# Optimization experiments

Measured on AMD Instinct MI355X. Metric: run time of the kernel, lower is better.

Reference implementation:

```python
import jax, jax.numpy as jnp
import numpy as np

B, S, D, H = 4, 2048, 1024, 16
DK = D // H  # d_k = d_v = 64


def setup_inputs() -> dict:
    key = jax.random.key(0)
    ks = jax.random.split(key, 9)
    sc = 0.02
    return {
        "x": jax.random.normal(ks[0], (B, S, D), dtype=jnp.float32),
        "Wq": jax.random.normal(ks[1], (H, D, DK), dtype=jnp.float32) * sc,
        "bq": jax.random.normal(ks[2], (H, DK), dtype=jnp.float32) * sc,
        "Wk": jax.random.normal(ks[3], (H, D, DK), dtype=jnp.float32) * sc,
        "bk": jax.random.normal(ks[4], (H, DK), dtype=jnp.float32) * sc,
        "Wv": jax.random.normal(ks[5], (H, D, DK), dtype=jnp.float32) * sc,
        "bv": jax.random.normal(ks[6], (H, DK), dtype=jnp.float32) * sc,
        "Wo": jax.random.normal(ks[7], (D, D), dtype=jnp.float32) * sc,
        "bo": jax.random.normal(ks[8], (D,), dtype=jnp.float32) * sc,
    }


def reference(x, Wq, bq, Wk, bk, Wv, bv, Wo, bo):
    # per-head learned projections (heads stacked on leading axis h)
    Q = jnp.einsum("bsd,hdk->bhsk", x, Wq) + bq[None, :, None, :]
    K = jnp.einsum("bsd,hdk->bhsk", x, Wk) + bk[None, :, None, :]
    V = jnp.einsum("bsd,hdk->bhsk", x, Wv) + bv[None, :, None, :]
    scores = jnp.einsum("bhsk,bhtk->bhst", Q, K) / jnp.sqrt(jnp.float32(DK))
    # causal mask: future_sight=0, past_sight=None -> positions t > s replaced by -1e9
    s_idx = jnp.arange(S)
    causal = s_idx[:, None] >= s_idx[None, :]  # [S, S] True where allowed
    scores = jnp.where(causal[None, None, :, :], scores, jnp.float32(-1e9))
    attn = jax.nn.softmax(scores, axis=-1)
    out = jnp.einsum("bhst,bhtk->bhsk", attn, V)  # [B, H, S, DK]
    # concat heads along feature dim (head order matches ModuleList order)
    cat = out.transpose(0, 2, 1, 3).reshape(B, S, D)
    return cat @ Wo + bo
```

## Files before the change

### kernel.cpp

```cpp
#include <hip/hip_runtime.h>
#include <stdint.h>

#define B_  4
#define S_  2048
#define D_  1024
#define H_  16
#define DK_ 64
#define M_  (B_ * S_)

typedef __attribute__((ext_vector_type(8))) short bf16x8;
typedef __attribute__((ext_vector_type(4))) float f32x4;

#define QSCALE 0.1803368801111204f

__device__ __forceinline__ uint16_t f2bf(float f) {
    uint32_t u = __builtin_bit_cast(uint32_t, f);
    u = (u + 0x7FFFu + ((u >> 16) & 1u)) >> 16;
    return (uint16_t)u;
}

__device__ __forceinline__ uint32_t pk2bf(float hi, float lo) {
    uint32_t a = __builtin_bit_cast(uint32_t, hi) + 0x8000u;
    uint32_t b = __builtin_bit_cast(uint32_t, lo) + 0x8000u;
    return __builtin_amdgcn_perm(a, b, 0x07060302u);
}

__global__ __launch_bounds__(256) void cvt_bf16_kernel(const float* __restrict__ in,
                                                       uint16_t* __restrict__ out, int n) {
    int i = (blockIdx.x * 256 + threadIdx.x) * 8;
    if (i >= n) return;
    float4 a = *(const float4*)&in[i];
    float4 b = *(const float4*)&in[i + 4];
    uint16_t o[8] = {f2bf(a.x), f2bf(a.y), f2bf(a.z), f2bf(a.w),
                     f2bf(b.x), f2bf(b.y), f2bf(b.z), f2bf(b.w)};
    *(uint4*)&out[i] = *(const uint4*)o;
}

__global__ __launch_bounds__(256) void transpose_cvt_qkv_kernel(
    const float* __restrict__ Wq, const float* __restrict__ Wk,
    const float* __restrict__ Wv, uint16_t* __restrict__ Wt) {
    __shared__ __align__(16) uint16_t tile[64][72];
    const int z = blockIdx.z;
    const int sel = z >> 4, mat = z & 15;
    const float* base = (sel == 0) ? Wq : (sel == 1) ? Wk : Wv;
    const float* inm = base + (size_t)mat * 1024 * 64;
    uint16_t* outm = Wt + (size_t)z * 65536;
    const int r0 = blockIdx.x * 64;
    const int t = threadIdx.x;
    const int lr = t >> 2, lc = (t & 3) * 16;
    uint16_t tmp[16];
    #pragma unroll
    for (int j = 0; j < 16; j += 4) {
        float4 v = *(const float4*)&inm[(size_t)(r0 + lr) * 64 + lc + j];
        tmp[j] = f2bf(v.x); tmp[j + 1] = f2bf(v.y); tmp[j + 2] = f2bf(v.z); tmp[j + 3] = f2bf(v.w);
    }
    *(uint4*)&tile[lr][lc]     = ((const uint4*)tmp)[0];
    *(uint4*)&tile[lr][lc + 8] = ((const uint4*)tmp)[1];
    __syncthreads();
    const int oc = t >> 2, orr = (t & 3) * 16;
    uint16_t ot[16];
    #pragma unroll
    for (int j = 0; j < 16; ++j) ot[j] = tile[orr + j][oc];
    *(uint4*)&outm[(size_t)oc * 1024 + r0 + orr]     = ((const uint4*)ot)[0];
    *(uint4*)&outm[(size_t)oc * 1024 + r0 + orr + 8] = ((const uint4*)ot)[1];
}

__global__ __launch_bounds__(256) void transpose_cvt_kernel(
    const float* __restrict__ in, uint16_t* __restrict__ out, int R, int C) {
    __shared__ __align__(16) uint16_t tile[64][72];
    const float* inm = in;
    uint16_t* outm = out;
    const int r0 = blockIdx.x * 64, c0 = blockIdx.y * 64;
    const int t = threadIdx.x;
    const int lr = t >> 2, lc = (t & 3) * 16;
    uint16_t tmp[16];
    #pragma unroll
    for (int j = 0; j < 16; j += 4) {
        float4 v = *(const float4*)&inm[(size_t)(r0 + lr) * C + c0 + lc + j];
        tmp[j] = f2bf(v.x); tmp[j + 1] = f2bf(v.y); tmp[j + 2] = f2bf(v.z); tmp[j + 3] = f2bf(v.w);
    }
    *(uint4*)&tile[lr][lc]     = ((const uint4*)tmp)[0];
    *(uint4*)&tile[lr][lc + 8] = ((const uint4*)tmp)[1];
    __syncthreads();
    const int oc = t >> 2, orr = (t & 3) * 16;
    uint16_t ot[16];
    #pragma unroll
    for (int j = 0; j < 16; ++j) ot[j] = tile[orr + j][oc];
    *(uint4*)&outm[(size_t)(c0 + oc) * R + r0 + orr]     = ((const uint4*)ot)[0];
    *(uint4*)&outm[(size_t)(c0 + oc) * R + r0 + orr + 8] = ((const uint4*)ot)[1];
}

__global__ __launch_bounds__(256) void qkv_mfma_kernel(
    const uint16_t* __restrict__ xb, const uint16_t* __restrict__ Wt,
    const float* __restrict__ bq, const float* __restrict__ bk, const float* __restrict__ bv,
    uint16_t* __restrict__ Q, uint16_t* __restrict__ K, uint16_t* __restrict__ V)
{
    __shared__ __align__(16) uint16_t As[128][72];
    __shared__ __align__(16) uint16_t Bs[128][72];
    const int tid = threadIdx.x;
    const int nb = blockIdx.x;
    const int sel = nb >> 3, npair = nb & 7;
    const int m0 = blockIdx.y * 128;
    const int lane = tid & 63, w = tid >> 6;
    const int wr = w >> 1, wc = w & 1;
    const int ll = lane & 15, quad = lane >> 4;

    const uint16_t* Bg = Wt + (size_t)nb * 128 * 1024;
    const float* bias = (sel == 0) ? bq : (sel == 1) ? bk : bv;

    const int ar = tid >> 1, ac = (tid & 1) * 32;

    f32x4 acc[4][4];
    const f32x4 zz = {0.f, 0.f, 0.f, 0.f};
    #pragma unroll
    for (int i = 0; i < 4; ++i)
        #pragma unroll
        for (int j = 0; j < 4; ++j) acc[i][j] = zz;

    for (int k0 = 0; k0 < 1024; k0 += 64) {
        __syncthreads();
        const uint16_t* ag = &xb[(size_t)(m0 + ar) * 1024 + k0 + ac];
        uint4 a0 = *(const uint4*)(ag);
        uint4 a1 = *(const uint4*)(ag + 8);
        uint4 a2 = *(const uint4*)(ag + 16);
        uint4 a3 = *(const uint4*)(ag + 24);
        const uint16_t* bg = &Bg[(size_t)ar * 1024 + k0 + ac];
        uint4 b0 = *(const uint4*)(bg);
        uint4 b1 = *(const uint4*)(bg + 8);
        uint4 b2 = *(const uint4*)(bg + 16);
        uint4 b3 = *(const uint4*)(bg + 24);
        *(uint4*)&As[ar][ac]      = a0;
        *(uint4*)&As[ar][ac + 8]  = a1;
        *(uint4*)&As[ar][ac + 16] = a2;
        *(uint4*)&As[ar][ac + 24] = a3;
        *(uint4*)&Bs[ar][ac]      = b0;
        *(uint4*)&Bs[ar][ac + 8]  = b1;
        *(uint4*)&Bs[ar][ac + 16] = b2;
        *(uint4*)&Bs[ar][ac + 24] = b3;
        __syncthreads();
        #pragma unroll
        for (int ks = 0; ks < 2; ++ks) {
            bf16x8 af[4], bfv[4];
            #pragma unroll
            for (int mt = 0; mt < 4; ++mt)
                af[mt] = *(const bf16x8*)&As[wr * 64 + mt * 16 + ll][ks * 32 + quad * 8];
            #pragma unroll
            for (int nt = 0; nt < 4; ++nt)
                bfv[nt] = *(const bf16x8*)&Bs[wc * 64 + nt * 16 + ll][ks * 32 + quad * 8];
            #pragma unroll
            for (int mt = 0; mt < 4; ++mt)
                #pragma unroll
                for (int nt = 0; nt < 4; ++nt)
                    acc[mt][nt] = __builtin_amdgcn_mfma_f32_16x16x32_bf16(af[mt], bfv[nt], acc[mt][nt], 0, 0, 0);
        }
    }

    if (sel == 2) {
        #pragma unroll
        for (int nt = 0; nt < 4; ++nt) {
            const int nl = wc * 64 + nt * 16 + ll;
            const int hh = npair * 2 + (nl >> 6);
            const int dk = nl & 63;
            const float bval = bias[npair * 128 + nl];
            #pragma unroll
            for (int mt = 0; mt < 4; ++mt) {
                int m = m0 + wr * 64 + mt * 16 + quad * 4;
                int b = m >> 11, s = m & 2047;
                uint2 pv;
                pv.x = pk2bf(acc[mt][nt][1] + bval, acc[mt][nt][0] + bval);
                pv.y = pk2bf(acc[mt][nt][3] + bval, acc[mt][nt][2] + bval);
                *(uint2*)&V[((size_t)(b * 16 + hh) * 64 + dk) * 2048 + s] = pv;
            }
        }
    } else {
        uint16_t* Out = (sel == 0) ? Q : K;
        const float qs = (sel == 0) ? QSCALE : 1.0f;
        #pragma unroll
        for (int nt = 0; nt < 4; ++nt) {
            const int nl = wc * 64 + nt * 16 + ll;
            const int hh = npair * 2 + (nl >> 6);
            const int dk = nl & 63;
            const float bval = bias[npair * 128 + nl];
            #pragma unroll
            for (int mt = 0; mt < 4; ++mt) {
                #pragma unroll
                for (int r = 0; r < 4; ++r) {
                    int m = m0 + wr * 64 + mt * 16 + quad * 4 + r;
                    int b = m >> 11, s = m & 2047;
                    float v = (acc[mt][nt][r] + bval) * qs;
                    Out[((size_t)(b * 16 + hh) * 2048 + s) * 64 + dk] = f2bf(v);
                }
            }
        }
    }
}

__global__ __launch_bounds__(256) void attn_mfma_kernel(
    const uint16_t* __restrict__ Q, const uint16_t* __restrict__ K,
    const uint16_t* __restrict__ Vg, uint16_t* __restrict__ CAT)
{
    __shared__ __align__(16) uint16_t Ks[64][72];
    __shared__ __align__(16) uint16_t Vt[64][72];
    __shared__ __align__(16) uint16_t Ps[128][72];

    const int tid = threadIdx.x;
    const int lane = tid & 63, w = tid >> 6;
    const int ll = lane & 15, quad = lane >> 4;
    const int p = blockIdx.x;
    const int bh = blockIdx.y;
    const int b = bh >> 4, h = bh & 15;

    const uint16_t* Qbh = Q + (size_t)bh * S_ * 64;
    const uint16_t* Kbh = K + (size_t)bh * S_ * 64;
    const uint16_t* Vbh = Vg + (size_t)bh * 64 * S_;
    uint16_t* Cbh = CAT + (size_t)b * 2048 * 1024 + h * 64;

    const int sr = tid >> 2, sc = (tid & 3) * 16;

    bf16x8 onesf;
    #pragma unroll
    for (int j = 0; j < 8; ++j) onesf[j] = (ll == 0) ? (short)0x3F80 : (short)0;

    const f32x4 zz = {0.f, 0.f, 0.f, 0.f};

    #pragma unroll 1
    for (int phase = 0; phase < 2; ++phase) {
        const int qtb = (phase == 0) ? (15 - p) : p;
        const int q0 = qtb * 128;
        const int qw = q0 + w * 32;

        bf16x8 qf[2][2];
        #pragma unroll
        for (int mt = 0; mt < 2; ++mt)
            #pragma unroll
            for (int ks = 0; ks < 2; ++ks)
                qf[mt][ks] = *(const bf16x8*)&Qbh[(size_t)(qw + mt * 16 + ll) * 64 + ks * 32 + quad * 8];

        f32x4 oacc[2][4];
        f32x4 lacc[2];
        #pragma unroll
        for (int i = 0; i < 2; ++i) {
            lacc[i] = zz;
            #pragma unroll
            for (int j = 0; j < 4; ++j) oacc[i][j] = zz;
        }

        const int ktmax = 2 * qtb + 1;

        for (int kt = 0; kt <= ktmax; ++kt) {
            const int tb = kt * 64;
            __syncthreads();
            {
                const uint16_t* g = &Kbh[(size_t)(tb + sr) * 64 + sc];
                uint4 v0 = *(const uint4*)g, v1 = *(const uint4*)(g + 8);
                *(uint4*)&Ks[sr][sc] = v0;
                *(uint4*)&Ks[sr][sc + 8] = v1;
            }
            {
                const uint16_t* g = &Vbh[(size_t)sr * 2048 + tb + sc];
                uint4 v0 = *(const uint4*)g, v1 = *(const uint4*)(g + 8);
                *(uint4*)&Vt[sr][sc] = v0;
                *(uint4*)&Vt[sr][sc + 8] = v1;
            }
            __syncthreads();

            const bool active = (tb <= qw + 31);
            if (active) {
                f32x4 sacc[4][2];
                #pragma unroll
                for (int i = 0; i < 4; ++i)
                    #pragma unroll
                    for (int j = 0; j < 2; ++j) sacc[i][j] = zz;
                #pragma unroll
                for (int ks = 0; ks < 2; ++ks) {
                    #pragma unroll
                    for (int tt = 0; tt < 4; ++tt) {
                        bf16x8 kf = *(const bf16x8*)&Ks[tt * 16 + ll][ks * 32 + quad * 8];
                        #pragma unroll
                        for (int mt = 0; mt < 2; ++mt)
                            sacc[tt][mt] = __builtin_amdgcn_mfma_f32_16x16x32_bf16(kf, qf[mt][ks], sacc[tt][mt], 0, 0, 0);
                    }
                }

                const bool needMask = (tb + 63 > qw);
                #pragma unroll
                for (int mt = 0; mt < 2; ++mt) {
                    const int qg = qw + mt * 16 + ll;
                    #pragma unroll
                    for (int tt = 0; tt < 4; ++tt) {
                        #pragma unroll
                        for (int r = 0; r < 4; ++r) {
                            float v = sacc[tt][mt][r];
                            if (needMask) {
                                int tg = tb + tt * 16 + quad * 4 + r;
                                v = (tg > qg) ? -1e30f : v;
                            }
                            sacc[tt][mt][r] = __builtin_amdgcn_exp2f(v);
                        }
                        uint2 pv;
                        pv.x = pk2bf(sacc[tt][mt][1], sacc[tt][mt][0]);
                        pv.y = pk2bf(sacc[tt][mt][3], sacc[tt][mt][2]);
                        *(uint2*)&Ps[w * 32 + mt * 16 + ll][tt * 16 + quad * 4] = pv;
                    }
                }

                #pragma unroll
                for (int ks = 0; ks < 2; ++ks) {
                    bf16x8 pf[2], vf[4];
                    #pragma unroll
                    for (int mt = 0; mt < 2; ++mt)
                        pf[mt] = *(const bf16x8*)&Ps[w * 32 + mt * 16 + ll][ks * 32 + quad * 8];
                    #pragma unroll
                    for (int nt = 0; nt < 4; ++nt)
                        vf[nt] = *(const bf16x8*)&Vt[nt * 16 + ll][ks * 32 + quad * 8];
                    #pragma unroll
                    for (int mt = 0; mt < 2; ++mt) {
                        lacc[mt] = __builtin_amdgcn_mfma_f32_16x16x32_bf16(pf[mt], onesf, lacc[mt], 0, 0, 0);
                        #pragma unroll
                        for (int nt = 0; nt < 4; ++nt)
                            oacc[mt][nt] = __builtin_amdgcn_mfma_f32_16x16x32_bf16(pf[mt], vf[nt], oacc[mt][nt], 0, 0, 0);
                    }
                }
            }
        }

        #pragma unroll
        for (int mt = 0; mt < 2; ++mt) {
            f32x4 li;
            #pragma unroll
            for (int r = 0; r < 4; ++r)
                li[r] = 1.0f / __shfl(lacc[mt][r], lane & 48);
            #pragma unroll
            for (int r = 0; r < 4; ++r) {
                int q = qw + mt * 16 + quad * 4 + r;
                #pragma unroll
                for (int nt = 0; nt < 4; ++nt) {
                    float v = oacc[mt][nt][r] * li[r];
                    Cbh[(size_t)q * 1024 + nt * 16 + ll] = f2bf(v);
                }
            }
        }
    }
}

__global__ __launch_bounds__(256) void oproj_mfma_kernel(
    const uint16_t* __restrict__ CATb, const uint16_t* __restrict__ Wot,
    const float* __restrict__ bo, float* __restrict__ out)
{
    __shared__ __align__(16) uint16_t As[128][72];
    __shared__ __align__(16) uint16_t Bs[128][72];
    const int tid = threadIdx.x;
    const int n0 = blockIdx.x * 128;
    const int m0 = blockIdx.y * 128;
    const int lane = tid & 63, w = tid >> 6;
    const int wr = w >> 1, wc = w & 1;
    const int ll = lane & 15, quad = lane >> 4;

    const int ar = tid >> 1, ac = (tid & 1) * 32;

    f32x4 acc[4][4];
    const f32x4 zz = {0.f, 0.f, 0.f, 0.f};
    #pragma unroll
    for (int i = 0; i < 4; ++i)
        #pragma unroll
        for (int j = 0; j < 4; ++j) acc[i][j] = zz;

    for (int k0 = 0; k0 < 1024; k0 += 64) {
        __syncthreads();
        const uint16_t* ag = &CATb[(size_t)(m0 + ar) * 1024 + k0 + ac];
        uint4 a0 = *(const uint4*)(ag);
        uint4 a1 = *(const uint4*)(ag + 8);
        uint4 a2 = *(const uint4*)(ag + 16);
        uint4 a3 = *(const uint4*)(ag + 24);
        const uint16_t* bg = &Wot[(size_t)(n0 + ar) * 1024 + k0 + ac];
        uint4 b0 = *(const uint4*)(bg);
        uint4 b1 = *(const uint4*)(bg + 8);
        uint4 b2 = *(const uint4*)(bg + 16);
        uint4 b3 = *(const uint4*)(bg + 24);
        *(uint4*)&As[ar][ac]      = a0;
        *(uint4*)&As[ar][ac + 8]  = a1;
        *(uint4*)&As[ar][ac + 16] = a2;
        *(uint4*)&As[ar][ac + 24] = a3;
        *(uint4*)&Bs[ar][ac]      = b0;
        *(uint4*)&Bs[ar][ac + 8]  = b1;
        *(uint4*)&Bs[ar][ac + 16] = b2;
        *(uint4*)&Bs[ar][ac + 24] = b3;
        __syncthreads();
        #pragma unroll
        for (int ks = 0; ks < 2; ++ks) {
            bf16x8 af[4], bfv[4];
            #pragma unroll
            for (int mt = 0; mt < 4; ++mt)
                af[mt] = *(const bf16x8*)&As[wr * 64 + mt * 16 + ll][ks * 32 + quad * 8];
            #pragma unroll
            for (int nt = 0; nt < 4; ++nt)
                bfv[nt] = *(const bf16x8*)&Bs[wc * 64 + nt * 16 + ll][ks * 32 + quad * 8];
            #pragma unroll
            for (int mt = 0; mt < 4; ++mt)
                #pragma unroll
                for (int nt = 0; nt < 4; ++nt)
                    acc[mt][nt] = __builtin_amdgcn_mfma_f32_16x16x32_bf16(af[mt], bfv[nt], acc[mt][nt], 0, 0, 0);
        }
    }

    #pragma unroll
    for (int nt = 0; nt < 4; ++nt) {
        const int nl = wc * 64 + nt * 16 + ll;
        const float bval = bo[n0 + nl];
        #pragma unroll
        for (int mt = 0; mt < 4; ++mt) {
            #pragma unroll
            for (int r = 0; r < 4; ++r) {
                int m = m0 + wr * 64 + mt * 16 + quad * 4 + r;
                out[(size_t)m * 1024 + n0 + nl] = acc[mt][nt][r] + bval;
            }
        }
    }
}

extern "C" void kernel_launch(void* const* d_in, const int* in_sizes, int n_in,
                              void* d_out, int out_size, void* d_ws, size_t ws_size,
                              hipStream_t stream) {
    const float* x  = (const float*)d_in[0];
    const float* Wq = (const float*)d_in[1];
    const float* bq = (const float*)d_in[2];
    const float* Wk = (const float*)d_in[3];
    const float* bk = (const float*)d_in[4];
    const float* Wv = (const float*)d_in[5];
    const float* bv = (const float*)d_in[6];
    const float* Wo = (const float*)d_in[7];
    const float* bo = (const float*)d_in[8];

    uint8_t* p = (uint8_t*)d_ws;
    uint16_t* xb   = (uint16_t*)p; p += (size_t)M_ * D_ * 2;
    uint16_t* Wt   = (uint16_t*)p; p += (size_t)3 * H_ * DK_ * D_ * 2;
    uint16_t* Wot  = (uint16_t*)p; p += (size_t)D_ * D_ * 2;
    uint16_t* Qb   = (uint16_t*)p; p += (size_t)B_ * H_ * S_ * DK_ * 2;
    uint16_t* Kb   = (uint16_t*)p; p += (size_t)B_ * H_ * S_ * DK_ * 2;
    uint16_t* Vb   = (uint16_t*)p; p += (size_t)B_ * H_ * S_ * DK_ * 2;
    uint16_t* CATb = (uint16_t*)p;

    cvt_bf16_kernel<<<dim3((M_ * D_) / 2048), 256, 0, stream>>>(x, xb, M_ * D_);
    transpose_cvt_qkv_kernel<<<dim3(16, 1, 48), 256, 0, stream>>>(Wq, Wk, Wv, Wt);
    transpose_cvt_kernel<<<dim3(D_ / 64, D_ / 64, 1), 256, 0, stream>>>(Wo, Wot, D_, D_);

    qkv_mfma_kernel<<<dim3(24, M_ / 128), 256, 0, stream>>>(xb, Wt, bq, bk, bv, Qb, Kb, Vb);
    attn_mfma_kernel<<<dim3(8, B_ * H_), 256, 0, stream>>>(Qb, Kb, Vb, CATb);
    oproj_mfma_kernel<<<dim3(8, M_ / 128), 256, 0, stream>>>(CATb, Wot, bo, (float*)d_out);
}
```

Baseline: 289.9 us.

## Use direct global-to-LDS loads, prefragmented weights, swizzled LDS, and one-tile attention blocks

Weights are repacked once into MFMA fragment order so each GEMM wave reads its B operand straight from global memory into registers, with no LDS staging for B. Activation, K and V tiles are loaded with global_load_lds into an XOR-swizzled LDS layout, which removes the register round trip and the padding. The attention grid changes from 8 blocks that each handle a paired short and long query tile to 16 blocks that each handle one tile, giving more parallelism but unbalanced per-block work. The risks are uncoalesced strided reads in the repack kernels and causal load imbalance across blocks.

```diff
diff --git a/kernel.cpp b/kernel.cpp
--- a/kernel.cpp
+++ b/kernel.cpp
@@ -23,6 +23,12 @@
     uint32_t a = __builtin_bit_cast(uint32_t, hi) + 0x8000u;
     uint32_t b = __builtin_bit_cast(uint32_t, lo) + 0x8000u;
     return __builtin_amdgcn_perm(a, b, 0x07060302u);
+}
+
+__device__ __forceinline__ void gl2lds16(const void* g, void* l) {
+    __builtin_amdgcn_global_load_lds(
+        (const __attribute__((address_space(1))) uint32_t*)g,
+        (__attribute__((address_space(3))) uint32_t*)l, 16, 0, 0);
 }
 
 __global__ __launch_bounds__(256) void cvt_bf16_kernel(const float* __restrict__ in,
@@ -36,67 +42,52 @@
     *(uint4*)&out[i] = *(const uint4*)o;
 }
 
-__global__ __launch_bounds__(256) void transpose_cvt_qkv_kernel(
+__global__ __launch_bounds__(256) void frag_qkv_kernel(
     const float* __restrict__ Wq, const float* __restrict__ Wk,
-    const float* __restrict__ Wv, uint16_t* __restrict__ Wt) {
-    __shared__ __align__(16) uint16_t tile[64][72];
-    const int z = blockIdx.z;
-    const int sel = z >> 4, mat = z & 15;
-    const float* base = (sel == 0) ? Wq : (sel == 1) ? Wk : Wv;
-    const float* inm = base + (size_t)mat * 1024 * 64;
-    uint16_t* outm = Wt + (size_t)z * 65536;
-    const int r0 = blockIdx.x * 64;
-    const int t = threadIdx.x;
-    const int lr = t >> 2, lc = (t & 3) * 16;
-    uint16_t tmp[16];
-    #pragma unroll
-    for (int j = 0; j < 16; j += 4) {
-        float4 v = *(const float4*)&inm[(size_t)(r0 + lr) * 64 + lc + j];
-        tmp[j] = f2bf(v.x); tmp[j + 1] = f2bf(v.y); tmp[j + 2] = f2bf(v.z); tmp[j + 3] = f2bf(v.w);
-    }
-    *(uint4*)&tile[lr][lc]     = ((const uint4*)tmp)[0];
-    *(uint4*)&tile[lr][lc + 8] = ((const uint4*)tmp)[1];
-    __syncthreads();
-    const int oc = t >> 2, orr = (t & 3) * 16;
-    uint16_t ot[16];
-    #pragma unroll
-    for (int j = 0; j < 16; ++j) ot[j] = tile[orr + j][oc];
-    *(uint4*)&outm[(size_t)oc * 1024 + r0 + orr]     = ((const uint4*)ot)[0];
-    *(uint4*)&outm[(size_t)oc * 1024 + r0 + orr + 8] = ((const uint4*)ot)[1];
-}
-
-__global__ __launch_bounds__(256) void transpose_cvt_kernel(
-    const float* __restrict__ in, uint16_t* __restrict__ out, int R, int C) {
-    __shared__ __align__(16) uint16_t tile[64][72];
-    const float* inm = in;
-    uint16_t* outm = out;
-    const int r0 = blockIdx.x * 64, c0 = blockIdx.y * 64;
-    const int t = threadIdx.x;
-    const int lr = t >> 2, lc = (t & 3) * 16;
-    uint16_t tmp[16];
-    #pragma unroll
-    for (int j = 0; j < 16; j += 4) {
-        float4 v = *(const float4*)&inm[(size_t)(r0 + lr) * C + c0 + lc + j];
-        tmp[j] = f2bf(v.x); tmp[j + 1] = f2bf(v.y); tmp[j + 2] = f2bf(v.z); tmp[j + 3] = f2bf(v.w);
-    }
-    *(uint4*)&tile[lr][lc]     = ((const uint4*)tmp)[0];
-    *(uint4*)&tile[lr][lc + 8] = ((const uint4*)tmp)[1];
-    __syncthreads();
-    const int oc = t >> 2, orr = (t & 3) * 16;
-    uint16_t ot[16];
-    #pragma unroll
-    for (int j = 0; j < 16; ++j) ot[j] = tile[orr + j][oc];
-    *(uint4*)&outm[(size_t)(c0 + oc) * R + r0 + orr]     = ((const uint4*)ot)[0];
-    *(uint4*)&outm[(size_t)(c0 + oc) * R + r0 + orr + 8] = ((const uint4*)ot)[1];
+    const float* __restrict__ Wv, uint16_t* __restrict__ Wtf) {
+    const int kb = blockIdx.x;
+    const int nb = blockIdx.y;
+    const int sel = nb >> 3, npair = nb & 7;
+    const float* W = (sel == 0) ? Wq : (sel == 1) ? Wk : Wv;
+    const int lane = threadIdx.x & 63, w = threadIdx.x >> 6;
+    const int ll = lane & 15, quad = lane >> 4;
+    #pragma unroll
+    for (int i = 0; i < 2; ++i) {
+        const int ntg = w + i * 4;
+        const int nl = ntg * 16 + ll;
+        const int h = npair * 2 + (nl >> 6), dk = nl & 63;
+        const float* src = W + ((size_t)h * 1024 + kb * 32 + quad * 8) * 64 + dk;
+        uint16_t tmp[8];
+        #pragma unroll
+        for (int j = 0; j < 8; ++j) tmp[j] = f2bf(src[(size_t)j * 64]);
+        *(uint4*)&Wtf[((((size_t)nb * 8 + ntg) * 32 + kb) * 64 + lane) * 8] = *(const uint4*)tmp;
+    }
+}
+
+__global__ __launch_bounds__(256) void frag_wo_kernel(
+    const float* __restrict__ Wo, uint16_t* __restrict__ Wof) {
+    const int kb = blockIdx.x;
+    const int nb2 = blockIdx.y;
+    const int lane = threadIdx.x & 63, w = threadIdx.x >> 6;
+    const int ll = lane & 15, quad = lane >> 4;
+    #pragma unroll
+    for (int i = 0; i < 2; ++i) {
+        const int ntg = w + i * 4;
+        const int n = nb2 * 128 + ntg * 16 + ll;
+        const float* src = Wo + (size_t)(kb * 32 + quad * 8) * 1024 + n;
+        uint16_t tmp[8];
+        #pragma unroll
+        for (int j = 0; j < 8; ++j) tmp[j] = f2bf(src[(size_t)j * 1024]);
+        *(uint4*)&Wof[((((size_t)nb2 * 8 + ntg) * 32 + kb) * 64 + lane) * 8] = *(const uint4*)tmp;
+    }
 }
 
 __global__ __launch_bounds__(256) void qkv_mfma_kernel(
-    const uint16_t* __restrict__ xb, const uint16_t* __restrict__ Wt,
+    const uint16_t* __restrict__ xb, const uint16_t* __restrict__ Wtf,
     const float* __restrict__ bq, const float* __restrict__ bk, const float* __restrict__ bv,
     uint16_t* __restrict__ Q, uint16_t* __restrict__ K, uint16_t* __restrict__ V)
 {
-    __shared__ __align__(16) uint16_t As[128][72];
-    __shared__ __align__(16) uint16_t Bs[128][72];
+    __shared__ uint16_t As[128 * 64];
     const int tid = threadIdx.x;
     const int nb = blockIdx.x;
     const int sel = nb >> 3, npair = nb & 7;
@@ -104,11 +95,13 @@
     const int lane = tid & 63, w = tid >> 6;
     const int wr = w >> 1, wc = w & 1;
     const int ll = lane & 15, quad = lane >> 4;
-
-    const uint16_t* Bg = Wt + (size_t)nb * 128 * 1024;
     const float* bias = (sel == 0) ? bq : (sel == 1) ? bk : bv;
 
-    const int ar = tid >> 1, ac = (tid & 1) * 32;
+    const int sr8 = lane >> 3;
+    const int scb = (lane & 7) ^ sr8;
+    uint16_t* aL = As + (size_t)(w * 4) * 512;
+
+    const size_t bfbase = (size_t)nb * 8 * 32 * 512 + (size_t)lane * 8;
 
     f32x4 acc[4][4];
     const f32x4 zz = {0.f, 0.f, 0.f, 0.f};
@@ -119,39 +112,31 @@
 
     for (int k0 = 0; k0 < 1024; k0 += 64) {
         __syncthreads();
-        const uint16_t* ag = &xb[(size_t)(m0 + ar) * 1024 + k0 + ac];
-        uint4 a0 = *(const uint4*)(ag);
-        uint4 a1 = *(const uint4*)(ag + 8);
-        uint4 a2 = *(const uint4*)(ag + 16);
-        uint4 a3 = *(const uint4*)(ag + 24);
-        const uint16_t* bg = &Bg[(size_t)ar * 1024 + k0 + ac];
-        uint4 b0 = *(const uint4*)(bg);
-        uint4 b1 = *(const uint4*)(bg + 8);
-        uint4 b2 = *(const uint4*)(bg + 16);
-        uint4 b3 = *(const uint4*)(bg + 24);
-        *(uint4*)&As[ar][ac]      = a0;
-        *(uint4*)&As[ar][ac + 8]  = a1;
-        *(uint4*)&As[ar][ac + 16] = a2;
-        *(uint4*)&As[ar][ac + 24] = a3;
-        *(uint4*)&Bs[ar][ac]      = b0;
-        *(uint4*)&Bs[ar][ac + 8]  = b1;
-        *(uint4*)&Bs[ar][ac + 16] = b2;
-        *(uint4*)&Bs[ar][ac + 24] = b3;
+        #pragma unroll
+        for (int i = 0; i < 4; ++i)
+            gl2lds16(xb + (size_t)(m0 + w * 32 + i * 8 + sr8) * 1024 + k0 + scb * 8,
+                     aL + i * 512);
+        bf16x8 bfv[2][4];
+        const int kb = k0 >> 5;
+        #pragma unroll
+        for (int ks = 0; ks < 2; ++ks)
+            #pragma unroll
+            for (int nt = 0; nt < 4; ++nt)
+                bfv[ks][nt] = *(const bf16x8*)&Wtf[bfbase + ((size_t)(wc * 4 + nt) * 32 + kb + ks) * 512];
         __syncthreads();
         #pragma unroll
         for (int ks = 0; ks < 2; ++ks) {
-            bf16x8 af[4], bfv[4];
+            bf16x8 af[4];
+            #pragma unroll
+            for (int mt = 0; mt < 4; ++mt) {
+                const int row = wr * 64 + mt * 16 + ll;
+                af[mt] = *(const bf16x8*)&As[row * 64 + (((ks * 4 + quad) ^ (ll & 7)) * 8)];
+            }
             #pragma unroll
             for (int mt = 0; mt < 4; ++mt)
-                af[mt] = *(const bf16x8*)&As[wr * 64 + mt * 16 + ll][ks * 32 + quad * 8];
-            #pragma unroll
-            for (int nt = 0; nt < 4; ++nt)
-                bfv[nt] = *(const bf16x8*)&Bs[wc * 64 + nt * 16 + ll][ks * 32 + quad * 8];
-            #pragma unroll
-            for (int mt = 0; mt < 4; ++mt)
                 #pragma unroll
                 for (int nt = 0; nt < 4; ++nt)
-                    acc[mt][nt] = __builtin_amdgcn_mfma_f32_16x16x32_bf16(af[mt], bfv[nt], acc[mt][nt], 0, 0, 0);
+                    acc[mt][nt] = __builtin_amdgcn_mfma_f32_16x16x32_bf16(af[mt], bfv[ks][nt], acc[mt][nt], 0, 0, 0);
         }
     }
 
@@ -199,14 +184,14 @@
     const uint16_t* __restrict__ Q, const uint16_t* __restrict__ K,
     const uint16_t* __restrict__ Vg, uint16_t* __restrict__ CAT)
 {
-    __shared__ __align__(16) uint16_t Ks[64][72];
-    __shared__ __align__(16) uint16_t Vt[64][72];
-    __shared__ __align__(16) uint16_t Ps[128][72];
+    __shared__ uint16_t Ks[64 * 64];
+    __shared__ uint16_t Vt[64 * 64];
+    __shared__ __align__(16) uint16_t Ps[128][68];
 
     const int tid = threadIdx.x;
     const int lane = tid & 63, w = tid >> 6;
     const int ll = lane & 15, quad = lane >> 4;
-    const int p = blockIdx.x;
+    const int qtb = 15 - (int)blockIdx.x;
     const int bh = blockIdx.y;
     const int b = bh >> 4, h = bh & 15;
 
@@ -215,148 +200,145 @@
     const uint16_t* Vbh = Vg + (size_t)bh * 64 * S_;
     uint16_t* Cbh = CAT + (size_t)b * 2048 * 1024 + h * 64;
 
-    const int sr = tid >> 2, sc = (tid & 3) * 16;
+    const int q0 = qtb * 128;
+    const int qw = q0 + w * 32;
+
+    const int sr8 = lane >> 3;
+    const int scb = (lane & 7) ^ sr8;
 
     bf16x8 onesf;
     #pragma unroll
     for (int j = 0; j < 8; ++j) onesf[j] = (ll == 0) ? (short)0x3F80 : (short)0;
 
+    bf16x8 qf[2][2];
+    #pragma unroll
+    for (int mt = 0; mt < 2; ++mt)
+        #pragma unroll
+        for (int ks = 0; ks < 2; ++ks)
+            qf[mt][ks] = *(const bf16x8*)&Qbh[(size_t)(qw + mt * 16 + ll) * 64 + ks * 32 + quad * 8];
+
     const f32x4 zz = {0.f, 0.f, 0.f, 0.f};
-
-    #pragma unroll 1
-    for (int phase = 0; phase < 2; ++phase) {
-        const int qtb = (phase == 0) ? (15 - p) : p;
-        const int q0 = qtb * 128;
-        const int qw = q0 + w * 32;
-
-        bf16x8 qf[2][2];
-        #pragma unroll
-        for (int mt = 0; mt < 2; ++mt)
-            #pragma unroll
-            for (int ks = 0; ks < 2; ++ks)
-                qf[mt][ks] = *(const bf16x8*)&Qbh[(size_t)(qw + mt * 16 + ll) * 64 + ks * 32 + quad * 8];
-
-        f32x4 oacc[2][4];
-        f32x4 lacc[2];
+    f32x4 oacc[2][4];
+    f32x4 lacc[2];
+    #pragma unroll
+    for (int i = 0; i < 2; ++i) {
+        lacc[i] = zz;
+        #pragma unroll
+        for (int j = 0; j < 4; ++j) oacc[i][j] = zz;
+    }
+
+    const int ktmax = 2 * qtb + 1;
+
+    for (int kt = 0; kt <= ktmax; ++kt) {
+        const int tb = kt * 64;
+        __syncthreads();
         #pragma unroll
         for (int i = 0; i < 2; ++i) {
-            lacc[i] = zz;
-            #pragma unroll
-            for (int j = 0; j < 4; ++j) oacc[i][j] = zz;
-        }
-
-        const int ktmax = 2 * qtb + 1;
-
-        for (int kt = 0; kt <= ktmax; ++kt) {
-            const int tb = kt * 64;
-            __syncthreads();
-            {
-                const uint16_t* g = &Kbh[(size_t)(tb + sr) * 64 + sc];
-                uint4 v0 = *(const uint4*)g, v1 = *(const uint4*)(g + 8);
-                *(uint4*)&Ks[sr][sc] = v0;
-                *(uint4*)&Ks[sr][sc + 8] = v1;
-            }
-            {
-                const uint16_t* g = &Vbh[(size_t)sr * 2048 + tb + sc];
-                uint4 v0 = *(const uint4*)g, v1 = *(const uint4*)(g + 8);
-                *(uint4*)&Vt[sr][sc] = v0;
-                *(uint4*)&Vt[sr][sc + 8] = v1;
-            }
-            __syncthreads();
-
-            const bool active = (tb <= qw + 31);
-            if (active) {
-                f32x4 sacc[4][2];
-                #pragma unroll
-                for (int i = 0; i < 4; ++i)
-                    #pragma unroll
-                    for (int j = 0; j < 2; ++j) sacc[i][j] = zz;
-                #pragma unroll
-                for (int ks = 0; ks < 2; ++ks) {
-                    #pragma unroll
-                    for (int tt = 0; tt < 4; ++tt) {
-                        bf16x8 kf = *(const bf16x8*)&Ks[tt * 16 + ll][ks * 32 + quad * 8];
-                        #pragma unroll
-                        for (int mt = 0; mt < 2; ++mt)
-                            sacc[tt][mt] = __builtin_amdgcn_mfma_f32_16x16x32_bf16(kf, qf[mt][ks], sacc[tt][mt], 0, 0, 0);
-                    }
-                }
-
-                const bool needMask = (tb + 63 > qw);
-                #pragma unroll
-                for (int mt = 0; mt < 2; ++mt) {
-                    const int qg = qw + mt * 16 + ll;
-                    #pragma unroll
-                    for (int tt = 0; tt < 4; ++tt) {
-                        #pragma unroll
-                        for (int r = 0; r < 4; ++r) {
-                            float v = sacc[tt][mt][r];
-                            if (needMask) {
-                                int tg = tb + tt * 16 + quad * 4 + r;
-                                v = (tg > qg) ? -1e30f : v;
-                            }
-                            sacc[tt][mt][r] = __builtin_amdgcn_exp2f(v);
-                        }
-                        uint2 pv;
-                        pv.x = pk2bf(sacc[tt][mt][1], sacc[tt][mt][0]);
-                        pv.y = pk2bf(sacc[tt][mt][3], sacc[tt][mt][2]);
-                        *(uint2*)&Ps[w * 32 + mt * 16 + ll][tt * 16 + quad * 4] = pv;
-                    }
-                }
-
-                #pragma unroll
-                for (int ks = 0; ks < 2; ++ks) {
-                    bf16x8 pf[2], vf[4];
+            const int c = w * 2 + i;
+            const int row = c * 8 + sr8;
+            gl2lds16(Kbh + (size_t)(tb + row) * 64 + scb * 8, Ks + (size_t)c * 512);
+            gl2lds16(Vbh + (size_t)row * 2048 + tb + scb * 8, Vt + (size_t)c * 512);
+        }
+        __syncthreads();
+
+        const bool active = (tb <= qw + 31);
+        if (active) {
+            f32x4 sacc[4][2];
+            #pragma unroll
+            for (int i = 0; i < 4; ++i)
+                #pragma unroll
+                for (int j = 0; j < 2; ++j) sacc[i][j] = zz;
+            #pragma unroll
+            for (int ks = 0; ks < 2; ++ks) {
+                #pragma unroll
+                for (int tt = 0; tt < 4; ++tt) {
+                    const int row = tt * 16 + ll;
+                    bf16x8 kf = *(const bf16x8*)&Ks[row * 64 + (((ks * 4 + quad) ^ (ll & 7)) * 8)];
                     #pragma unroll
                     for (int mt = 0; mt < 2; ++mt)
-                        pf[mt] = *(const bf16x8*)&Ps[w * 32 + mt * 16 + ll][ks * 32 + quad * 8];
+                        sacc[tt][mt] = __builtin_amdgcn_mfma_f32_16x16x32_bf16(kf, qf[mt][ks], sacc[tt][mt], 0, 0, 0);
+                }
+            }
+
+            const bool needMask = (tb + 63 > qw);
+            #pragma unroll
+            for (int mt = 0; mt < 2; ++mt) {
+                const int qg = qw + mt * 16 + ll;
+                #pragma unroll
+                for (int tt = 0; tt < 4; ++tt) {
+                    #pragma unroll
+                    for (int r = 0; r < 4; ++r) {
+                        float v = sacc[tt][mt][r];
+                        if (needMask) {
+                            int tg = tb + tt * 16 + quad * 4 + r;
+                            v = (tg > qg) ? -1e30f : v;
+                        }
+                        sacc[tt][mt][r] = __builtin_amdgcn_exp2f(v);
+                    }
+                    uint2 pv;
+                    pv.x = pk2bf(sacc[tt][mt][1], sacc[tt][mt][0]);
+                    pv.y = pk2bf(sacc[tt][mt][3], sacc[tt][mt][2]);
+                    *(uint2*)&Ps[w * 32 + mt * 16 + ll][tt * 16 + quad * 4] = pv;
+                }
+            }
+
+            #pragma unroll
+            for (int ks = 0; ks < 2; ++ks) {
+                bf16x8 pf[2], vf[4];
+                #pragma unroll
+                for (int mt = 0; mt < 2; ++mt)
+                    pf[mt] = *(const bf16x8*)&Ps[w * 32 + mt * 16 + ll][ks * 32 + quad * 8];
+                #pragma unroll
+                for (int nt = 0; nt < 4; ++nt) {
+                    const int row = nt * 16 + ll;
+                    vf[nt] = *(const bf16x8*)&Vt[row * 64 + (((ks * 4 + quad) ^ (ll & 7)) * 8)];
+                }
+                #pragma unroll
+                for (int mt = 0; mt < 2; ++mt) {
+                    lacc[mt] = __builtin_amdgcn_mfma_f32_16x16x32_bf16(pf[mt], onesf, lacc[mt], 0, 0, 0);
                     #pragma unroll
                     for (int nt = 0; nt < 4; ++nt)
-                        vf[nt] = *(const bf16x8*)&Vt[nt * 16 + ll][ks * 32 + quad * 8];
-                    #pragma unroll
-                    for (int mt = 0; mt < 2; ++mt) {
-                        lacc[mt] = __builtin_amdgcn_mfma_f32_16x16x32_bf16(pf[mt], onesf, lacc[mt], 0, 0, 0);
-                        #pragma unroll
-                        for (int nt = 0; nt < 4; ++nt)
-                            oacc[mt][nt] = __builtin_amdgcn_mfma_f32_16x16x32_bf16(pf[mt], vf[nt], oacc[mt][nt], 0, 0, 0);
-                    }
+                        oacc[mt][nt] = __builtin_amdgcn_mfma_f32_16x16x32_bf16(pf[mt], vf[nt], oacc[mt][nt], 0, 0, 0);
                 }
             }
         }
-
-        #pragma unroll
-        for (int mt = 0; mt < 2; ++mt) {
-            f32x4 li;
-            #pragma unroll
-            for (int r = 0; r < 4; ++r)
-                li[r] = 1.0f / __shfl(lacc[mt][r], lane & 48);
-            #pragma unroll
-            for (int r = 0; r < 4; ++r) {
-                int q = qw + mt * 16 + quad * 4 + r;
-                #pragma unroll
-                for (int nt = 0; nt < 4; ++nt) {
-                    float v = oacc[mt][nt][r] * li[r];
-                    Cbh[(size_t)q * 1024 + nt * 16 + ll] = f2bf(v);
-                }
+    }
+
+    #pragma unroll
+    for (int mt = 0; mt < 2; ++mt) {
+        f32x4 li;
+        #pragma unroll
+        for (int r = 0; r < 4; ++r)
+            li[r] = 1.0f / __shfl(lacc[mt][r], lane & 48);
+        #pragma unroll
+        for (int r = 0; r < 4; ++r) {
+            int q = qw + mt * 16 + quad * 4 + r;
+            #pragma unroll
+            for (int nt = 0; nt < 4; ++nt) {
+                float v = oacc[mt][nt][r] * li[r];
+                Cbh[(size_t)q * 1024 + nt * 16 + ll] = f2bf(v);
             }
         }
     }
 }
 
 __global__ __launch_bounds__(256) void oproj_mfma_kernel(
-    const uint16_t* __restrict__ CATb, const uint16_t* __restrict__ Wot,
+    const uint16_t* __restrict__ CATb, const uint16_t* __restrict__ Wof,
     const float* __restrict__ bo, float* __restrict__ out)
 {
-    __shared__ __align__(16) uint16_t As[128][72];
-    __shared__ __align__(16) uint16_t Bs[128][72];
+    __shared__ uint16_t As[128 * 64];
     const int tid = threadIdx.x;
-    const int n0 = blockIdx.x * 128;
+    const int nb2 = blockIdx.x;
     const int m0 = blockIdx.y * 128;
     const int lane = tid & 63, w = tid >> 6;
     const int wr = w >> 1, wc = w & 1;
     const int ll = lane & 15, quad = lane >> 4;
 
-    const int ar = tid >> 1, ac = (tid & 1) * 32;
+    const int sr8 = lane >> 3;
+    const int scb = (lane & 7) ^ sr8;
+    uint16_t* aL = As + (size_t)(w * 4) * 512;
+
+    const size_t bfbase = (size_t)nb2 * 8 * 32 * 512 + (size_t)lane * 8;
 
     f32x4 acc[4][4];
     const f32x4 zz = {0.f, 0.f, 0.f, 0.f};
@@ -367,52 +349,44 @@
 
     for (int k0 = 0; k0 < 1024; k0 += 64) {
         __syncthreads();
-        const uint16_t* ag = &CATb[(size_t)(m0 + ar) * 1024 + k0 + ac];
-        uint4 a0 = *(const uint4*)(ag);
-        uint4 a1 = *(const uint4*)(ag + 8);
-        uint4 a2 = *(const uint4*)(ag + 16);
-        uint4 a3 = *(const uint4*)(ag + 24);
-        const uint16_t* bg = &Wot[(size_t)(n0 + ar) * 1024 + k0 + ac];
-        uint4 b0 = *(const uint4*)(bg);
-        uint4 b1 = *(const uint4*)(bg + 8);
-        uint4 b2 = *(const uint4*)(bg + 16);
-        uint4 b3 = *(const uint4*)(bg + 24);
-        *(uint4*)&As[ar][ac]      = a0;
-        *(uint4*)&As[ar][ac + 8]  = a1;
-        *(uint4*)&As[ar][ac + 16] = a2;
-        *(uint4*)&As[ar][ac + 24] = a3;
-        *(uint4*)&Bs[ar][ac]      = b0;
-        *(uint4*)&Bs[ar][ac + 8]  = b1;
-        *(uint4*)&Bs[ar][ac + 16] = b2;
-        *(uint4*)&Bs[ar][ac + 24] = b3;
+        #pragma unroll
+        for (int i = 0; i < 4; ++i)
+            gl2lds16(CATb + (size_t)(m0 + w * 32 + i * 8 + sr8) * 1024 + k0 + scb * 8,
+                     aL + i * 512);
+        bf16x8 bfv[2][4];
+        const int kb = k0 >> 5;
+        #pragma unroll
+        for (int ks = 0; ks < 2; ++ks)
+            #pragma unroll
+            for (int nt = 0; nt < 4; ++nt)
+                bfv[ks][nt] = *(const bf16x8*)&Wof[bfbase + ((size_t)(wc * 4 + nt) * 32 + kb + ks) * 512];
         __syncthreads();
         #pragma unroll
         for (int ks = 0; ks < 2; ++ks) {
-            bf16x8 af[4], bfv[4];
+            bf16x8 af[4];
+            #pragma unroll
+            for (int mt = 0; mt < 4; ++mt) {
+                const int row = wr * 64 + mt * 16 + ll;
+                af[mt] = *(const bf16x8*)&As[row * 64 + (((ks * 4 + quad) ^ (ll & 7)) * 8)];
+            }
             #pragma unroll
             for (int mt = 0; mt < 4; ++mt)
-                af[mt] = *(const bf16x8*)&As[wr * 64 + mt * 16 + ll][ks * 32 + quad * 8];
-            #pragma unroll
-            for (int nt = 0; nt < 4; ++nt)
-                bfv[nt] = *(const bf16x8*)&Bs[wc * 64 + nt * 16 + ll][ks * 32 + quad * 8];
-            #pragma unroll
-            for (int mt = 0; mt < 4; ++mt)
                 #pragma unroll
                 for (int nt = 0; nt < 4; ++nt)
-                    acc[mt][nt] = __builtin_amdgcn_mfma_f32_16x16x32_bf16(af[mt], bfv[nt], acc[mt][nt], 0, 0, 0);
+                    acc[mt][nt] = __builtin_amdgcn_mfma_f32_16x16x32_bf16(af[mt], bfv[ks][nt], acc[mt][nt], 0, 0, 0);
         }
     }
 
     #pragma unroll
     for (int nt = 0; nt < 4; ++nt) {
         const int nl = wc * 64 + nt * 16 + ll;
-        const float bval = bo[n0 + nl];
+        const float bval = bo[nb2 * 128 + nl];
         #pragma unroll
         for (int mt = 0; mt < 4; ++mt) {
             #pragma unroll
             for (int r = 0; r < 4; ++r) {
                 int m = m0 + wr * 64 + mt * 16 + quad * 4 + r;
-                out[(size_t)m * 1024 + n0 + nl] = acc[mt][nt][r] + bval;
+                out[(size_t)m * 1024 + nb2 * 128 + nl] = acc[mt][nt][r] + bval;
             }
         }
     }
@@ -433,18 +407,18 @@
 
     uint8_t* p = (uint8_t*)d_ws;
     uint16_t* xb   = (uint16_t*)p; p += (size_t)M_ * D_ * 2;
-    uint16_t* Wt   = (uint16_t*)p; p += (size_t)3 * H_ * DK_ * D_ * 2;
-    uint16_t* Wot  = (uint16_t*)p; p += (size_t)D_ * D_ * 2;
+    uint16_t* Wtf  = (uint16_t*)p; p += (size_t)3 * H_ * DK_ * D_ * 2;
+    uint16_t* Wof  = (uint16_t*)p; p += (size_t)D_ * D_ * 2;
     uint16_t* Qb   = (uint16_t*)p; p += (size_t)B_ * H_ * S_ * DK_ * 2;
     uint16_t* Kb   = (uint16_t*)p; p += (size_t)B_ * H_ * S_ * DK_ * 2;
     uint16_t* Vb   = (uint16_t*)p; p += (size_t)B_ * H_ * S_ * DK_ * 2;
     uint16_t* CATb = (uint16_t*)p;
 
     cvt_bf16_kernel<<<dim3((M_ * D_) / 2048), 256, 0, stream>>>(x, xb, M_ * D_);
-    transpose_cvt_qkv_kernel<<<dim3(16, 1, 48), 256, 0, stream>>>(Wq, Wk, Wv, Wt);
-    transpose_cvt_kernel<<<dim3(D_ / 64, D_ / 64, 1), 256, 0, stream>>>(Wo, Wot, D_, D_);
-
-    qkv_mfma_kernel<<<dim3(24, M_ / 128), 256, 0, stream>>>(xb, Wt, bq, bk, bv, Qb, Kb, Vb);
-    attn_mfma_kernel<<<dim3(8, B_ * H_), 256, 0, stream>>>(Qb, Kb, Vb, CATb);
-    oproj_mfma_kernel<<<dim3(8, M_ / 128), 256, 0, stream>>>(CATb, Wot, bo, (float*)d_out);
-}
+    frag_qkv_kernel<<<dim3(32, 24), 256, 0, stream>>>(Wq, Wk, Wv, Wtf);
+    frag_wo_kernel<<<dim3(32, 8), 256, 0, stream>>>(Wo, Wof);
+
+    qkv_mfma_kernel<<<dim3(24, M_ / 128), 256, 0, stream>>>(xb, Wtf, bq, bk, bv, Qb, Kb, Vb);
+    attn_mfma_kernel<<<dim3(16, B_ * H_), 256, 0, stream>>>(Qb, Kb, Vb, CATb);
+    oproj_mfma_kernel<<<dim3(8, M_ / 128), 256, 0, stream>>>(CATb, Wof, bo, (float*)d_out);
+}
```

Result: slower. 322.9 us (+11.4%).
